# Optimization experiments

Hardware: AMD Instinct MI355X
Metric: run time of the kernel (lower is better)

The kernel has to match this reference:

```python
import jax, jax.numpy as jnp
import numpy as np

N_NODES = 50000
N_EDGES = 800000
D_NODE = 64
D_EDGE = 64
HIDDEN = 128


def setup_inputs() -> dict:
    key = jax.random.key(0)
    k1, k2, k3, k4, k5 = jax.random.split(key, 5)
    x_node = jax.random.normal(k1, (N_NODES, D_NODE), dtype=jnp.float32)
    x_edge = jax.random.normal(k2, (N_EDGES, D_EDGE), dtype=jnp.float32)
    edge_index = jax.random.randint(k3, (2, N_EDGES), 0, N_NODES, dtype=jnp.int64)
    d_in = D_NODE + D_EDGE
    W1 = jax.random.normal(k4, (d_in, HIDDEN), dtype=jnp.float32) / np.sqrt(d_in)
    b1 = jnp.zeros((HIDDEN,), dtype=jnp.float32)
    W2 = jax.random.normal(k5, (HIDDEN, D_NODE), dtype=jnp.float32) / np.sqrt(HIDDEN)
    b2 = jnp.zeros((D_NODE,), dtype=jnp.float32)
    return {"x_node": x_node, "x_edge": x_edge, "edge_index": edge_index,
            "W1": W1, "b1": b1, "W2": W2, "b2": b2}


def reference(x_node, x_edge, edge_index, W1, b1, W2, b2):
    # Both scatter_adds accumulate into the SAME buffer: sum of edge features
    # indexed by src (edge_index[0]) plus by dst (edge_index[1]).
    agg = jnp.zeros((x_node.shape[0], x_edge.shape[1]), dtype=x_edge.dtype)
    agg = agg.at[edge_index[0]].add(x_edge)
    agg = agg.at[edge_index[1]].add(x_edge)
    h = jnp.concatenate([x_node, agg], axis=1)          # [N, d_node + d_edge]
    h = jax.nn.relu(h @ W1 + b1)                        # [N, hidden]
    x_node_ = h @ W2 + b2                               # [N, d_node]
    return x_node_
```

## Files before the change

kernel.cpp:

```cpp
#include <hip/hip_runtime.h>

#define D 64
#define HID 128
#define MLPB 1024
#define WPB 16
#define NB 8
#define CAP 96
#define WIN_SHIFT 12

typedef unsigned short ush;

__device__ __forceinline__ ush f2bf(float f)
{
    unsigned u = __float_as_uint(f);
    return (ush)((u + 0x7FFF + ((u >> 16) & 1)) >> 16);
}
__device__ __forceinline__ float bf_lo(unsigned p) { return __uint_as_float(p << 16); }
__device__ __forceinline__ float bf_hi(unsigned p) { return __uint_as_float(p & 0xFFFF0000u); }

__device__ __forceinline__ bool detect_i64(const int* __restrict__ eidx, int lane)
{
    int probe = eidx[2 * lane + 1];
    return (__ballot(probe == 0) == ~0ULL);
}

__global__ __launch_bounds__(256)
void p0_nid(const int* __restrict__ eidx, ush* __restrict__ nid,
            int* __restrict__ counts, int n_zero, int n_edges)
{
    const int t = blockIdx.x * 256 + threadIdx.x;
    const bool is64 = detect_i64(eidx, threadIdx.x & 63);
    const int E2 = 2 * n_edges;
    if (t < E2) nid[t] = (ush)(is64 ? eidx[2 * (size_t)t] : eidx[t]);
    if (t < n_zero) counts[t] = 0;
}

__global__ __launch_bounds__(256)
void p1_place16(const ush* __restrict__ nid, int* __restrict__ counts,
                int* __restrict__ elist, int* __restrict__ ovf_cnt,
                int2* __restrict__ ovf, int n_edges)
{
    const int lo = blockIdx.y << WIN_SHIFT;
    const int hi = lo + (1 << WIN_SHIFT);
    const int E2 = 2 * n_edges;
    const int stride = gridDim.x * 256;
    for (int t = blockIdx.x * 256 + threadIdx.x; t < E2; t += stride) {
        int idx = nid[t];
        if (idx >= lo && idx < hi) {
            int eid = (t < n_edges) ? t : t - n_edges;
            int c = atomicAdd(&counts[idx], 1);
            if (c < CAP) elist[(size_t)idx * CAP + c] = eid;
            else {
                int p = atomicAdd(ovf_cnt, 1);
                ovf[p] = make_int2(idx, eid);
            }
        }
    }
}

__global__ __launch_bounds__(256)
void p1_place(const int* __restrict__ eidx, int* __restrict__ counts,
              int* __restrict__ elist, int* __restrict__ ovf_cnt,
              int2* __restrict__ ovf, int n_edges)
{
    const int lo = blockIdx.y << WIN_SHIFT;
    const int hi = lo + (1 << WIN_SHIFT);
    const int E2 = 2 * n_edges;
    const bool is64 = detect_i64(eidx, threadIdx.x & 63);
    const int stride = gridDim.x * 256;
    for (int t = blockIdx.x * 256 + threadIdx.x; t < E2; t += stride) {
        int idx = is64 ? eidx[2 * (size_t)t] : eidx[t];
        if (idx >= lo && idx < hi) {
            int eid = (t < n_edges) ? t : t - n_edges;
            int c = atomicAdd(&counts[idx], 1);
            if (c < CAP) elist[(size_t)idx * CAP + c] = eid;
            else {
                int p = atomicAdd(ovf_cnt, 1);
                ovf[p] = make_int2(idx, eid);
            }
        }
    }
}

__global__ __launch_bounds__(256)
void p2_gather(const float* __restrict__ x_edge, const int* __restrict__ counts,
               const int* __restrict__ elist, float* __restrict__ agg, int n_nodes)
{
    const int w = (blockIdx.x * 256 + threadIdx.x) >> 6;
    if (w >= n_nodes) return;
    const int lane = threadIdx.x & 63;
    const int sub = lane >> 4;
    const int q   = lane & 15;
    const float4* __restrict__ xe4 = (const float4*)x_edge;

    int cnt = counts[w]; if (cnt > CAP) cnt = CAP;
    const int beg = w * CAP, end = beg + cnt;
    float4 acc = make_float4(0.f, 0.f, 0.f, 0.f);

    int i = beg + sub;
    for (; i + 12 < end; i += 16) {
        int e0 = elist[i];
        int e1 = elist[i + 4];
        int e2 = elist[i + 8];
        int e3 = elist[i + 12];
        float4 v0 = xe4[(size_t)e0 * 16 + q];
        float4 v1 = xe4[(size_t)e1 * 16 + q];
        float4 v2 = xe4[(size_t)e2 * 16 + q];
        float4 v3 = xe4[(size_t)e3 * 16 + q];
        acc.x += (v0.x + v1.x) + (v2.x + v3.x);
        acc.y += (v0.y + v1.y) + (v2.y + v3.y);
        acc.z += (v0.z + v1.z) + (v2.z + v3.z);
        acc.w += (v0.w + v1.w) + (v2.w + v3.w);
    }
    for (; i < end; i += 4) {
        float4 v = xe4[(size_t)elist[i] * 16 + q];
        acc.x += v.x; acc.y += v.y; acc.z += v.z; acc.w += v.w;
    }

    #pragma unroll
    for (int m = 16; m < 64; m <<= 1) {
        acc.x += __shfl_xor(acc.x, m);
        acc.y += __shfl_xor(acc.y, m);
        acc.z += __shfl_xor(acc.z, m);
        acc.w += __shfl_xor(acc.w, m);
    }
    if (sub == 0)
        ((float4*)agg)[(size_t)w * 16 + q] = acc;
}

__global__ __launch_bounds__(256)
void p3_ovf(const float* __restrict__ x_edge, const int* __restrict__ ovf_cnt,
            const int2* __restrict__ ovf, float* __restrict__ agg)
{
    const int n = *ovf_cnt;
    const int lane = threadIdx.x & 63;
    const int wv = (blockIdx.x * 256 + threadIdx.x) >> 6;
    const int nw = gridDim.x * 4;
    for (int i = wv; i < n; i += nw) {
        int2 p = ovf[i];
        float v = x_edge[(size_t)p.y * D + lane];
        unsafeAtomicAdd(&agg[(size_t)p.x * D + lane], v);
    }
}

__global__ __launch_bounds__(256)
void nb_scatter(const float* __restrict__ x_edge, const int* __restrict__ eidx,
                float* __restrict__ agg, int n_edges)
{
    long long t = (long long)blockIdx.x * 256 + threadIdx.x;
    int e = (int)(t >> 6);
    if (e >= n_edges) return;
    int d = (int)(t & 63);
    bool is64 = detect_i64(eidx, threadIdx.x & 63);
    int s, dd;
    if (is64) {
        s  = eidx[2 * (size_t)e];
        dd = eidx[2 * ((size_t)n_edges + (size_t)e)];
    } else {
        s  = eidx[e];
        dd = eidx[n_edges + e];
    }
    float v = x_edge[(size_t)e * D + d];
    unsafeAtomicAdd(&agg[(size_t)s * D + d], v);
    unsafeAtomicAdd(&agg[(size_t)dd * D + d], v);
}

__global__ __launch_bounds__(MLPB, 1)
void p4_mlp(const float* __restrict__ x_node, const float* __restrict__ agg,
            const float* __restrict__ W1, const float* __restrict__ b1,
            const float* __restrict__ W2, const float* __restrict__ b2,
            float* __restrict__ out, int n_nodes)
{
    __shared__ float2   sW1p[HID * 64];
    __shared__ unsigned sW2p[64 * 64];
    __shared__ float    sb1[HID];
    __shared__ float    sb2[D];
    __shared__ float4   s_buf[WPB][128][2];

    {
        for (int t = threadIdx.x; t < HID * 64; t += MLPB) {
            int k = t >> 6, j = t & 63;
            sW1p[t] = make_float2(W1[k * HID + j], W1[k * HID + 64 + j]);
        }
        for (int t = threadIdx.x; t < 64 * 64; t += MLPB) {
            int q = t >> 6, j = t & 63;
            unsigned lo = f2bf(W2[(2 * q) * D + j]);
            unsigned hi = f2bf(W2[(2 * q + 1) * D + j]);
            sW2p[t] = lo | (hi << 16);
        }
        if (threadIdx.x < 128) sb1[threadIdx.x] = b1[threadIdx.x];
        else if (threadIdx.x < 192) sb2[threadIdx.x - 128] = b2[threadIdx.x - 128];
    }
    __syncthreads();

    const int wave = threadIdx.x >> 6;
    const int lane = threadIdx.x & 63;
    const int group = blockIdx.x * WPB + wave;
    const int ngroups = gridDim.x * WPB;
    const int nbatches = (n_nodes + NB - 1) / NB;

    const float bh0 = sb1[lane], bh1 = sb1[64 + lane];
    const float bo  = sb2[lane];

    for (int g = group; g < nbatches; g += ngroups) {
        const int n0 = g * NB;

        float vx[NB], va[NB];
        #pragma unroll
        for (int b = 0; b < NB; ++b) {
            const int n = n0 + b;
            const bool ok = (n < n_nodes);
            vx[b] = ok ? x_node[(size_t)n * D + lane] : 0.f;
            va[b] = ok ? agg[(size_t)n * D + lane] : 0.f;
        }
        s_buf[wave][lane][0]      = make_float4(vx[0], vx[1], vx[2], vx[3]);
        s_buf[wave][lane][1]      = make_float4(vx[4], vx[5], vx[6], vx[7]);
        s_buf[wave][64 + lane][0] = make_float4(va[0], va[1], va[2], va[3]);
        s_buf[wave][64 + lane][1] = make_float4(va[4], va[5], va[6], va[7]);
        __builtin_amdgcn_wave_barrier();

        float a0[NB], a1[NB];
        #pragma unroll
        for (int b = 0; b < NB; ++b) { a0[b] = bh0; a1[b] = bh1; }

        #pragma unroll 2
        for (int k = 0; k < 128; ++k) {
            const float4 A0 = s_buf[wave][k][0];
            const float4 A1 = s_buf[wave][k][1];
            const float2 w  = sW1p[k * 64 + lane];
            a0[0] = fmaf(A0.x, w.x, a0[0]); a1[0] = fmaf(A0.x, w.y, a1[0]);
            a0[1] = fmaf(A0.y, w.x, a0[1]); a1[1] = fmaf(A0.y, w.y, a1[1]);
            a0[2] = fmaf(A0.z, w.x, a0[2]); a1[2] = fmaf(A0.z, w.y, a1[2]);
            a0[3] = fmaf(A0.w, w.x, a0[3]); a1[3] = fmaf(A0.w, w.y, a1[3]);
            a0[4] = fmaf(A1.x, w.x, a0[4]); a1[4] = fmaf(A1.x, w.y, a1[4]);
            a0[5] = fmaf(A1.y, w.x, a0[5]); a1[5] = fmaf(A1.y, w.y, a1[5]);
            a0[6] = fmaf(A1.z, w.x, a0[6]); a1[6] = fmaf(A1.z, w.y, a1[6]);
            a0[7] = fmaf(A1.w, w.x, a0[7]); a1[7] = fmaf(A1.w, w.y, a1[7]);
        }
        __builtin_amdgcn_wave_barrier();
        s_buf[wave][lane][0] = make_float4(fmaxf(a0[0], 0.f), fmaxf(a0[1], 0.f),
                                           fmaxf(a0[2], 0.f), fmaxf(a0[3], 0.f));
        s_buf[wave][lane][1] = make_float4(fmaxf(a0[4], 0.f), fmaxf(a0[5], 0.f),
                                           fmaxf(a0[6], 0.f), fmaxf(a0[7], 0.f));
        s_buf[wave][64 + lane][0] = make_float4(fmaxf(a1[0], 0.f), fmaxf(a1[1], 0.f),
                                                fmaxf(a1[2], 0.f), fmaxf(a1[3], 0.f));
        s_buf[wave][64 + lane][1] = make_float4(fmaxf(a1[4], 0.f), fmaxf(a1[5], 0.f),
                                                fmaxf(a1[6], 0.f), fmaxf(a1[7], 0.f));
        __builtin_amdgcn_wave_barrier();

        float o[NB];
        #pragma unroll
        for (int b = 0; b < NB; ++b) o[b] = bo;
        #pragma unroll 2
        for (int q2 = 0; q2 < 64; ++q2) {
            const unsigned wp = sW2p[q2 * 64 + lane];
            const float w0 = bf_lo(wp), w1 = bf_hi(wp);
            const float4 H0a = s_buf[wave][2 * q2][0];
            const float4 H0b = s_buf[wave][2 * q2][1];
            const float4 H1a = s_buf[wave][2 * q2 + 1][0];
            const float4 H1b = s_buf[wave][2 * q2 + 1][1];
            o[0] = fmaf(H0a.x, w0, o[0]); o[0] = fmaf(H1a.x, w1, o[0]);
            o[1] = fmaf(H0a.y, w0, o[1]); o[1] = fmaf(H1a.y, w1, o[1]);
            o[2] = fmaf(H0a.z, w0, o[2]); o[2] = fmaf(H1a.z, w1, o[2]);
            o[3] = fmaf(H0a.w, w0, o[3]); o[3] = fmaf(H1a.w, w1, o[3]);
            o[4] = fmaf(H0b.x, w0, o[4]); o[4] = fmaf(H1b.x, w1, o[4]);
            o[5] = fmaf(H0b.y, w0, o[5]); o[5] = fmaf(H1b.y, w1, o[5]);
            o[6] = fmaf(H0b.z, w0, o[6]); o[6] = fmaf(H1b.z, w1, o[6]);
            o[7] = fmaf(H0b.w, w0, o[7]); o[7] = fmaf(H1b.w, w1, o[7]);
        }
        #pragma unroll
        for (int b = 0; b < NB; ++b) {
            const int n = n0 + b;
            if (n < n_nodes) out[(size_t)n * D + lane] = o[b];
        }
    }
}

extern "C" void kernel_launch(void* const* d_in, const int* in_sizes, int n_in,
                              void* d_out, int out_size, void* d_ws, size_t ws_size,
                              hipStream_t stream)
{
    const float* x_node = (const float*)d_in[0];
    const float* x_edge = (const float*)d_in[1];
    const int*   eidx   = (const int*)d_in[2];
    const float* W1     = (const float*)d_in[3];
    const float* b1     = (const float*)d_in[4];
    const float* W2     = (const float*)d_in[5];
    const float* b2     = (const float*)d_in[6];
    float* out = (float*)d_out;

    const int n_nodes = in_sizes[0] / D;
    const int n_edges = in_sizes[2] / 2;
    const int E2 = 2 * n_edges;

    float* agg = out;

    const size_t w_counts = (size_t)n_nodes;
    const size_t w_ovfc   = w_counts + 1;
    const size_t w_ovf    = (w_ovfc + 1 + 1) & ~(size_t)1;
    const size_t w_elist  = w_ovf + (size_t)E2 * 2;
    const size_t w_nid    = w_elist + (size_t)n_nodes * CAP;
    const size_t w_total  = w_nid + ((size_t)E2 + 1) / 2;
    const size_t need     = w_total * 4;
    const bool u16_ok     = (n_nodes <= 65535);

    if (ws_size >= need) {
        int*  counts  = (int*)d_ws;
        int*  ovf_cnt = (int*)d_ws + w_ovfc;
        int2* ovf     = (int2*)((int*)d_ws + w_ovf);
        int*  elist   = (int*)d_ws + w_elist;
        ush*  nid     = (ush*)((int*)d_ws + w_nid);

        const int n_windows = (n_nodes + (1 << WIN_SHIFT) - 1) >> WIN_SHIFT;

        if (u16_ok) {
            p0_nid<<<(E2 + 255) / 256, 256, 0, stream>>>(
                eidx, nid, counts, n_nodes + 2, n_edges);
            p1_place16<<<dim3(512, n_windows), 256, 0, stream>>>(
                nid, counts, elist, ovf_cnt, ovf, n_edges);
        } else {
            hipMemsetAsync(counts, 0, ((size_t)n_nodes + 2) * 4, stream);
            p1_place<<<dim3(512, n_windows), 256, 0, stream>>>(
                eidx, counts, elist, ovf_cnt, ovf, n_edges);
        }

        p2_gather<<<(n_nodes * 64 + 255) / 256, 256, 0, stream>>>(
            x_edge, counts, elist, agg, n_nodes);

        p3_ovf<<<64, 256, 0, stream>>>(x_edge, ovf_cnt, ovf, agg);
    } else {
        hipMemsetAsync(agg, 0, (size_t)n_nodes * D * sizeof(float), stream);
        long long threads = (long long)n_edges * 64;
        nb_scatter<<<(int)((threads + 255) / 256), 256, 0, stream>>>(
            x_edge, eidx, agg, n_edges);
    }

    p4_mlp<<<196, MLPB, 0, stream>>>(x_node, agg, W1, b1, W2, b2, out, n_nodes);
}
```

Before: 199.9 us.

## Fuse aggregation phases into one cooperative kernel with grid syncs

Replaces the four separate aggregation launches (index narrowing, windowed placement, gather, overflow) with a single cooperative persistent kernel that separates the phases with grid-wide syncs. The aim is to remove kernel launch gaps and tail effects between phases. The persistent grid is sized by occupancy, so each phase runs with fewer threads than the original launches. The placement loop now scans every edge once per window in grid-stride fashion, which repeats the full index read for each window. The kernel also adds per-call device attribute and occupancy queries on the host.

```diff
diff --git a/kernel.cpp b/kernel.cpp
--- a/kernel.cpp
+++ b/kernel.cpp
@@ -1,4 +1,7 @@
 #include <hip/hip_runtime.h>
+#include <hip/hip_cooperative_groups.h>
+
+namespace cg = cooperative_groups;
 
 #define D 64
 #define HID 128
@@ -22,6 +25,107 @@
 {
     int probe = eidx[2 * lane + 1];
     return (__ballot(probe == 0) == ~0ULL);
+}
+
+__global__ __launch_bounds__(256)
+void fused_agg(const int* __restrict__ eidx, ush* __restrict__ nid,
+               int* __restrict__ zbase, int* __restrict__ counts,
+               int* __restrict__ elist, int* __restrict__ ovf_cnt,
+               int2* __restrict__ ovf, const float* __restrict__ x_edge,
+               float* __restrict__ agg, int n_edges, int n_nodes, int u16_ok)
+{
+    cg::grid_group grid = cg::this_grid();
+    const int E2 = 2 * n_edges;
+    const int tid = blockIdx.x * 256 + threadIdx.x;
+    const int nthreads = gridDim.x * 256;
+    const bool is64 = detect_i64(eidx, threadIdx.x & 63);
+
+    if (u16_ok) {
+        for (int t = tid; t < E2; t += nthreads)
+            nid[t] = (ush)(is64 ? eidx[2 * (size_t)t] : eidx[t]);
+    }
+    for (int t = tid; t < n_nodes + 2; t += nthreads) zbase[t] = 0;
+    grid.sync();
+
+    const int nwin = (n_nodes + (1 << WIN_SHIFT) - 1) >> WIN_SHIFT;
+    for (int wi = 0; wi < nwin; ++wi) {
+        const int lo = wi << WIN_SHIFT;
+        const int hi = lo + (1 << WIN_SHIFT);
+        for (int t = tid; t < E2; t += nthreads) {
+            int idx = u16_ok ? (int)nid[t]
+                             : (is64 ? eidx[2 * (size_t)t] : eidx[t]);
+            if (idx >= lo && idx < hi) {
+                int eid = (t < n_edges) ? t : t - n_edges;
+                int c = atomicAdd(&counts[idx], 1);
+                if (c < CAP) elist[(size_t)idx * CAP + c] = eid;
+                else {
+                    int p = atomicAdd(ovf_cnt, 1);
+                    ovf[p] = make_int2(idx, eid);
+                }
+            }
+        }
+    }
+    grid.sync();
+
+    {
+        const int lane = threadIdx.x & 63;
+        const int sub = lane >> 4;
+        const int q   = lane & 15;
+        const float4* __restrict__ xe4 = (const float4*)x_edge;
+        const int wave0 = tid >> 6;
+        const int nwaves = nthreads >> 6;
+
+        for (int w = wave0; w < n_nodes; w += nwaves) {
+            int cnt = counts[w]; if (cnt > CAP) cnt = CAP;
+            const int beg = w * CAP, end = beg + cnt;
+            float4 acc = make_float4(0.f, 0.f, 0.f, 0.f);
+
+            int i = beg + sub;
+            for (; i + 12 < end; i += 16) {
+                int e0 = elist[i];
+                int e1 = elist[i + 4];
+                int e2 = elist[i + 8];
+                int e3 = elist[i + 12];
+                float4 v0 = xe4[(size_t)e0 * 16 + q];
+                float4 v1 = xe4[(size_t)e1 * 16 + q];
+                float4 v2 = xe4[(size_t)e2 * 16 + q];
+                float4 v3 = xe4[(size_t)e3 * 16 + q];
+                acc.x += (v0.x + v1.x) + (v2.x + v3.x);
+                acc.y += (v0.y + v1.y) + (v2.y + v3.y);
+                acc.z += (v0.z + v1.z) + (v2.z + v3.z);
+                acc.w += (v0.w + v1.w) + (v2.w + v3.w);
+            }
+            for (; i < end; i += 4) {
+                float4 v = xe4[(size_t)elist[i] * 16 + q];
+                acc.x += v.x; acc.y += v.y; acc.z += v.z; acc.w += v.w;
+            }
+
+            #pragma unroll
+            for (int m = 16; m < 64; m <<= 1) {
+                acc.x += __shfl_xor(acc.x, m);
+                acc.y += __shfl_xor(acc.y, m);
+                acc.z += __shfl_xor(acc.z, m);
+                acc.w += __shfl_xor(acc.w, m);
+            }
+            if (sub == 0)
+                ((float4*)agg)[(size_t)w * 16 + q] = acc;
+        }
+    }
+    grid.sync();
+
+    {
+        const int n = *ovf_cnt;
+        if (n > 0) {
+            const int lane = threadIdx.x & 63;
+            const int wave0 = tid >> 6;
+            const int nwaves = nthreads >> 6;
+            for (int i = wave0; i < n; i += nwaves) {
+                int2 p = ovf[i];
+                float v = x_edge[(size_t)p.y * D + lane];
+                unsafeAtomicAdd(&agg[(size_t)p.x * D + lane], v);
+            }
+        }
+    }
 }
 
 __global__ __launch_bounds__(256)
@@ -116,7 +220,6 @@
         float4 v = xe4[(size_t)elist[i] * 16 + q];
         acc.x += v.x; acc.y += v.y; acc.z += v.z; acc.w += v.w;
     }
-
     #pragma unroll
     for (int m = 16; m < 64; m <<= 1) {
         acc.x += __shfl_xor(acc.x, m);
@@ -302,7 +405,7 @@
     const size_t w_nid    = w_elist + (size_t)n_nodes * CAP;
     const size_t w_total  = w_nid + ((size_t)E2 + 1) / 2;
     const size_t need     = w_total * 4;
-    const bool u16_ok     = (n_nodes <= 65535);
+    const int u16_ok      = (n_nodes <= 65535) ? 1 : 0;
 
     if (ws_size >= need) {
         int*  counts  = (int*)d_ws;
@@ -311,23 +414,47 @@
         int*  elist   = (int*)d_ws + w_elist;
         ush*  nid     = (ush*)((int*)d_ws + w_nid);
 
-        const int n_windows = (n_nodes + (1 << WIN_SHIFT) - 1) >> WIN_SHIFT;
-
-        if (u16_ok) {
-            p0_nid<<<(E2 + 255) / 256, 256, 0, stream>>>(
-                eidx, nid, counts, n_nodes + 2, n_edges);
-            p1_place16<<<dim3(512, n_windows), 256, 0, stream>>>(
-                nid, counts, elist, ovf_cnt, ovf, n_edges);
+        int dev = 0; hipGetDevice(&dev);
+        int coop = 0;
+        hipDeviceGetAttribute(&coop, hipDeviceAttributeCooperativeLaunch, dev);
+        int ncu = 0;
+        hipDeviceGetAttribute(&ncu, hipDeviceAttributeMultiprocessorCount, dev);
+        int nblk = 0;
+        if (coop)
+            hipOccupancyMaxActiveBlocksPerMultiprocessor(
+                &nblk, (const void*)fused_agg, 256, 0);
+
+        if (coop && nblk > 0 && ncu > 0) {
+            const int grid = ncu * nblk;
+            const int*   a_eidx  = eidx;   ush*  a_nid  = nid;
+            int*  a_zbase = counts;        int*  a_cnts = counts;
+            int*  a_elist = elist;         int*  a_ovfc = ovf_cnt;
+            int2* a_ovf   = ovf;           const float* a_xe = x_edge;
+            float* a_agg  = agg;
+            int a_E = n_edges, a_N = n_nodes, a_u16 = u16_ok;
+            void* args[] = { (void*)&a_eidx, (void*)&a_nid, (void*)&a_zbase,
+                             (void*)&a_cnts, (void*)&a_elist, (void*)&a_ovfc,
+                             (void*)&a_ovf, (void*)&a_xe, (void*)&a_agg,
+                             (void*)&a_E, (void*)&a_N, (void*)&a_u16 };
+            hipLaunchCooperativeKernel((const void*)fused_agg,
+                                       dim3(grid), dim3(256),
+                                       args, 0, stream);
         } else {
-            hipMemsetAsync(counts, 0, ((size_t)n_nodes + 2) * 4, stream);
-            p1_place<<<dim3(512, n_windows), 256, 0, stream>>>(
-                eidx, counts, elist, ovf_cnt, ovf, n_edges);
-        }
-
-        p2_gather<<<(n_nodes * 64 + 255) / 256, 256, 0, stream>>>(
-            x_edge, counts, elist, agg, n_nodes);
-
-        p3_ovf<<<64, 256, 0, stream>>>(x_edge, ovf_cnt, ovf, agg);
+            const int n_windows = (n_nodes + (1 << WIN_SHIFT) - 1) >> WIN_SHIFT;
+            if (u16_ok) {
+                p0_nid<<<(E2 + 255) / 256, 256, 0, stream>>>(
+                    eidx, nid, counts, n_nodes + 2, n_edges);
+                p1_place16<<<dim3(512, n_windows), 256, 0, stream>>>(
+                    nid, counts, elist, ovf_cnt, ovf, n_edges);
+            } else {
+                hipMemsetAsync(counts, 0, ((size_t)n_nodes + 2) * 4, stream);
+                p1_place<<<dim3(512, n_windows), 256, 0, stream>>>(
+                    eidx, counts, elist, ovf_cnt, ovf, n_edges);
+            }
+            p2_gather<<<(n_nodes * 64 + 255) / 256, 256, 0, stream>>>(
+                x_edge, counts, elist, agg, n_nodes);
+            p3_ovf<<<64, 256, 0, stream>>>(x_edge, ovf_cnt, ovf, agg);
+        }
     } else {
         hipMemsetAsync(agg, 0, (size_t)n_nodes * D * sizeof(float), stream);
         long long threads = (long long)n_edges * 64;
```

Measured after the change: 605.0 us. 3.03x slower.
